# Optimization experiments

Hardware: AMD Instinct MI355X
Metric: run time of the kernel (lower is better)

The kernel has to match this reference:

```python
import jax, jax.numpy as jnp
import numpy as np

B, N = 8, 256          # trees per batch, nodes per tree
H, E, RD = 512, 512, 64  # hidden, word-embed, relation-embed dims
V, R = 32000, 64       # word vocab, relation vocab
SOS = 0                # SOS / null-token word id


def setup_inputs() -> dict:
    key = jax.random.key(0)
    ks = jax.random.split(key, 10)
    rng = np.random.default_rng(0)
    # topologically ordered tree: parent[i] < i, parent[0] = -1 (root -> encoder state)
    parent = np.full((N,), -1, dtype=np.int32)
    for i in range(1, N):
        parent[i] = rng.integers(0, i)
    s = 0.02
    return {
        "rel_ids": jax.random.randint(ks[0], (B, N), 0, R, dtype=jnp.int32),
        "sent_ids": jax.random.randint(ks[1], (B, N), 0, V, dtype=jnp.int32),
        "parent": jnp.asarray(parent),
        "root_h": jax.random.normal(ks[2], (B, H), jnp.float32),
        "word_emb": jax.random.normal(ks[3], (V, E), jnp.float32) * s,
        "rel_emb": jax.random.normal(ks[4], (R, RD), jnp.float32) * s,
        "Wx": jax.random.normal(ks[5], (RD + E, 4 * H), jnp.float32) * s,
        "Wh": jax.random.normal(ks[6], (H, 4 * H), jnp.float32) * s,
        "b": jnp.zeros((4 * H,), jnp.float32),
        "Wo": jax.random.normal(ks[7], (H, V), jnp.float32) * s,
        "bo": jnp.zeros((V,), jnp.float32),
    }


def reference(rel_ids, sent_ids, parent, root_h, word_emb, rel_emb, Wx, Wh, b, Wo, bo):
    Bd, Nd = rel_ids.shape
    Hd = root_h.shape[1]
    # word fed to each node = gold word of its parent (teacher forcing); SOS at root
    pidx = jnp.maximum(parent, 0)                           # [N]
    pword = jnp.where(parent[None, :] < 0, SOS, sent_ids[:, pidx])  # [B,N]
    x = jnp.concatenate([rel_emb[rel_ids], word_emb[pword]], axis=-1)  # [B,N,RD+E]
    Xg = jnp.einsum('bnd,dg->bng', x, Wx) + b               # precomputed input gates [B,N,4H]
    slot = parent + 1                                       # state-store slot (0 = root state)

    Hs0 = jnp.zeros((Bd, Nd + 1, Hd), Xg.dtype).at[:, 0].set(root_h)
    Cs0 = Hs0  # original sets cell state = hidden at the root

    def step(carry, inp):
        Hs, Cs = carry
        xg, sl, i = inp
        ph, pc = Hs[:, sl], Cs[:, sl]                       # parent state [B,H]
        g = xg + ph @ Wh                                    # [B,4H]
        ig, fg, og, gg = jnp.split(g, 4, axis=-1)
        c = jax.nn.sigmoid(fg) * pc + jax.nn.sigmoid(ig) * jnp.tanh(gg)
        h = jax.nn.sigmoid(og) * jnp.tanh(c)
        Hs = Hs.at[:, i + 1].set(h)
        Cs = Cs.at[:, i + 1].set(c)
        return (Hs, Cs), h

    xs = (Xg.transpose(1, 0, 2), slot, jnp.arange(Nd))
    (_, _), hs = jax.lax.scan(step, (Hs0, Cs0), xs)         # hs: [N,B,H]
    hs = hs.transpose(1, 0, 2)                              # [B,N,H]
    logits = jnp.einsum('bnh,hv->bnv', hs, Wo) + bo         # per-node vocab logits
    return logits
```

## Files before the change

kernel.cpp:

```cpp
#include <hip/hip_runtime.h>
#include <hip/hip_bf16.h>
#include <stdint.h>

#define BB 8
#define NN 256
#define HH 512
#define G4 2048
#define EE 512
#define RDIM 64
#define KX 576
#define VV 32000
#define SLICES 64
#define CSTRIDE 16

using f32x4 = __attribute__((ext_vector_type(4))) float;
using bf16x8 = __attribute__((ext_vector_type(8))) short;

__device__ __forceinline__ unsigned short f2bf(float f) {
  unsigned int u = __float_as_uint(f);
  u = (u + 0x7FFFu + ((u >> 16) & 1u)) >> 16;
  return (unsigned short)u;
}
__device__ __forceinline__ float bf2f(unsigned short s) {
  return __uint_as_float(((unsigned int)s) << 16);
}
__device__ __forceinline__ float sigm(float x) { return 1.0f / (1.0f + __expf(-x)); }

__global__ void init_kernel(const float* __restrict__ root_h, float* __restrict__ Hs,
                            float* __restrict__ Cs) {
  int i = blockIdx.x * 256 + threadIdx.x;
  float v = root_h[i];
  Hs[i] = v;
  Cs[i] = v;
}

__global__ __launch_bounds__(64) void levels_kernel(const int* __restrict__ parent,
                                                    int* __restrict__ order) {
  __shared__ int dep[NN];
  __shared__ int cnt[NN];
  int tid = threadIdx.x;
  for (int i = tid; i < NN; i += 64) cnt[i] = 0;
  __syncthreads();
  if (tid == 0) {
    for (int i = 0; i < NN; ++i) {
      int p = parent[i];
      int d = (p < 0) ? 0 : dep[p] + 1;
      dep[i] = d;
      cnt[d]++;
    }
    int run = 0;
    for (int d = 0; d < NN; ++d) { int c = cnt[d]; cnt[d] = run; run += c; }
    for (int i = 0; i < NN; ++i) order[cnt[dep[i]]++] = i;
  }
}

__global__ __launch_bounds__(256) void xg_kernel(
    const int* __restrict__ rel_ids, const int* __restrict__ sent_ids,
    const int* __restrict__ parent, const float* __restrict__ word_emb,
    const float* __restrict__ rel_emb, const float* __restrict__ Wx,
    const float* __restrict__ bias, float* __restrict__ Xg) {
  int n = blockIdx.y;
  int cb = blockIdx.x;
  int tid = threadIdx.x;
  __shared__ float xs[BB * KX];
  int par = parent[n];
  int b = tid >> 5;
  int l32 = tid & 31;
  int rid = rel_ids[b * NN + n];
  int pw = (par < 0) ? 0 : sent_ids[b * NN + par];
  const float* re = rel_emb + (size_t)rid * RDIM;
  const float* we = word_emb + (size_t)pw * EE;
  for (int q = l32; q < RDIM; q += 32) xs[b * KX + q] = re[q];
  for (int q = l32; q < EE; q += 32) xs[b * KX + RDIM + q] = we[q];
  __syncthreads();
  int col = cb * 256 + tid;
  float bb = bias[col];
  float acc[BB];
#pragma unroll
  for (int i = 0; i < BB; ++i) acc[i] = bb;
  const float* wxp = Wx + col;
  for (int k = 0; k < KX; k += 4) {
    float w0 = wxp[(size_t)(k + 0) * G4];
    float w1 = wxp[(size_t)(k + 1) * G4];
    float w2 = wxp[(size_t)(k + 2) * G4];
    float w3 = wxp[(size_t)(k + 3) * G4];
#pragma unroll
    for (int i = 0; i < BB; ++i) {
      f32x4 p = *(const f32x4*)&xs[i * KX + k];
      acc[i] = fmaf(p[0], w0, acc[i]);
      acc[i] = fmaf(p[1], w1, acc[i]);
      acc[i] = fmaf(p[2], w2, acc[i]);
      acc[i] = fmaf(p[3], w3, acc[i]);
    }
  }
  float* xgout = Xg + (size_t)n * (BB * G4) + col;
#pragma unroll
  for (int i = 0; i < BB; ++i) xgout[(size_t)i * G4] = acc[i];
}

__global__ __launch_bounds__(256) void wot_kernel(const float* __restrict__ Wo,
                                                  unsigned short* __restrict__ WoT) {
  __shared__ float t[64][65];
  int n0 = blockIdx.x * 64;
  int k0 = blockIdx.y * 64;
  int tid = threadIdx.x;
  int c = tid & 63;
  int r4 = tid >> 6;
#pragma unroll
  for (int i = 0; i < 16; ++i) {
    int r = r4 * 16 + i;
    t[r][c] = Wo[(size_t)(k0 + r) * VV + n0 + c];
  }
  __syncthreads();
#pragma unroll
  for (int i = 0; i < 16; ++i) {
    int nr = r4 * 16 + i;
    WoT[(size_t)(n0 + nr) * HH + k0 + c] = f2bf(t[c][nr]);
  }
}

__global__ __launch_bounds__(256, 3) void scan_kernel(
    const int* __restrict__ parent, const float* __restrict__ Wh,
    const float* __restrict__ Xg, float* Hs, float* Cs,
    unsigned short* __restrict__ hs_bf, const int* __restrict__ order,
    int* count, int* abortf, int ngroups) {
  int bid = blockIdx.x;
  int s = bid & 63;
  int g = bid >> 6;
  int tid = threadIdx.x;
  int lc = tid & 31;
  int kseg = tid >> 5;
  int b_ = tid >> 3, h_ = tid & 7;

  __shared__ __align__(16) unsigned short WhL[32 * 512];
  __shared__ __align__(16) float phL[BB * HH];

  for (int q = tid; q < 32 * 512; q += 256) {
    int k = q >> 5, c = q & 31;
    int gc = (c >> 3) * HH + s * 8 + (c & 7);
    WhL[((k >> 3) * 32 + c) * 8 + (k & 7)] = f2bf(Wh[(size_t)k * G4 + gc]);
  }
  __syncthreads();

  for (int idx = g; idx < NN; idx += ngroups) {
    int node = order[idx];
    int slot = parent[node] + 1;
    float xg4[4];
    if (tid < 64) {
#pragma unroll
      for (int gt = 0; gt < 4; ++gt)
        xg4[gt] = Xg[(size_t)node * (BB * G4) + (size_t)b_ * G4 + gt * HH + s * 8 + h_];
    }
    if (tid == 0 && slot > 0) {
      int v = 0;
      for (long spin = 0; spin < 150000L; ++spin) {
        v = __hip_atomic_load(&count[(size_t)(slot - 1) * CSTRIDE],
                              __ATOMIC_RELAXED, __HIP_MEMORY_SCOPE_AGENT);
        if (v == SLICES) break;
        if ((spin & 1023) == 1023) {
          if (__hip_atomic_load(abortf, __ATOMIC_RELAXED,
                                __HIP_MEMORY_SCOPE_AGENT) != 0) break;
        }
        __builtin_amdgcn_s_sleep(2);
      }
      if (v != SLICES) {
        __hip_atomic_store(abortf, 1, __ATOMIC_RELAXED, __HIP_MEMORY_SCOPE_AGENT);
      }
    }
    __syncthreads();

    {
      int b = tid >> 5, ko = (tid & 31) * 16;
      unsigned long long* src =
          (unsigned long long*)(Hs + (size_t)slot * (BB * HH) + b * HH + ko);
      float* d = &phL[b * HH + ko];
#pragma unroll
      for (int j = 0; j < 8; ++j) {
        unsigned long long v = __hip_atomic_load(&src[j], __ATOMIC_RELAXED,
                                                 __HIP_MEMORY_SCOPE_AGENT);
        d[2 * j] = __uint_as_float((unsigned int)v);
        d[2 * j + 1] = __uint_as_float((unsigned int)(v >> 32));
      }
    }
    __syncthreads();

    float acc[8];
#pragma unroll
    for (int b = 0; b < 8; ++b) acc[b] = 0.f;
    for (int k8 = 0; k8 < 8; ++k8) {
      int kg = kseg * 8 + k8;
      int kloc = kg * 8;
      bf16x8 wv = *(const bf16x8*)&WhL[(kg * 32 + lc) * 8];
      float wf[8];
#pragma unroll
      for (int j = 0; j < 8; ++j) wf[j] = bf2f((unsigned short)wv[j]);
#pragma unroll
      for (int b = 0; b < 8; ++b) {
        const float* pp = &phL[b * HH + kloc];
        f32x4 p0 = *(const f32x4*)pp;
        f32x4 p1 = *(const f32x4*)(pp + 4);
        acc[b] = fmaf(p0[0], wf[0], acc[b]);
        acc[b] = fmaf(p0[1], wf[1], acc[b]);
        acc[b] = fmaf(p0[2], wf[2], acc[b]);
        acc[b] = fmaf(p0[3], wf[3], acc[b]);
        acc[b] = fmaf(p1[0], wf[4], acc[b]);
        acc[b] = fmaf(p1[1], wf[5], acc[b]);
        acc[b] = fmaf(p1[2], wf[6], acc[b]);
        acc[b] = fmaf(p1[3], wf[7], acc[b]);
      }
    }
    __syncthreads();
    {
      float* part = phL;
      *(f32x4*)&part[tid * 8] = (f32x4){acc[0], acc[1], acc[2], acc[3]};
      *(f32x4*)&part[tid * 8 + 4] = (f32x4){acc[4], acc[5], acc[6], acc[7]};
    }
    __syncthreads();
    if (tid < 64) {
      const float* part = phL;
      float gsum[4];
#pragma unroll
      for (int gt = 0; gt < 4; ++gt) {
        int lc2 = gt * 8 + h_;
        float sm = xg4[gt];
#pragma unroll
        for (int q = 0; q < 8; ++q) sm += part[(q * 32 + lc2) * 8 + b_];
        gsum[gt] = sm;
      }
      int hidx = s * 8 + h_;
      float pc = __hip_atomic_load(&Cs[(size_t)slot * (BB * HH) + b_ * HH + hidx],
                                   __ATOMIC_RELAXED, __HIP_MEMORY_SCOPE_AGENT);
      float c = sigm(gsum[1]) * pc + sigm(gsum[0]) * tanhf(gsum[3]);
      float h = sigm(gsum[2]) * tanhf(c);
      size_t oi = (size_t)(node + 1) * (BB * HH) + b_ * HH + hidx;
      __hip_atomic_store(&Cs[oi], c, __ATOMIC_RELAXED, __HIP_MEMORY_SCOPE_AGENT);
      __hip_atomic_store(&Hs[oi], h, __ATOMIC_RELAXED, __HIP_MEMORY_SCOPE_AGENT);
      hs_bf[((size_t)b_ * NN + node) * HH + hidx] = f2bf(h);
    }
    if (tid == 0) {
      asm volatile("s_waitcnt vmcnt(0)" ::: "memory");
      __hip_atomic_fetch_add(&count[(size_t)node * CSTRIDE], 1, __ATOMIC_RELAXED,
                             __HIP_MEMORY_SCOPE_AGENT);
    }
    __syncthreads();
  }
}

__global__ __launch_bounds__(256) void gemm_kernel(
    const unsigned short* __restrict__ A, const unsigned short* __restrict__ Bt,
    const float* __restrict__ bo, float* __restrict__ C) {
  int bid = blockIdx.x;
  int swz = (bid & 7) * 500 + (bid >> 3);
  int nt = swz >> 4;
  int mt = swz & 15;
  int tid = threadIdx.x;
  int wave = tid >> 6;
  int lane = tid & 63;
  int wr = wave >> 1, wc = wave & 1;
  int lr = lane & 15, lh = lane >> 4;
  __shared__ __align__(16) unsigned short Al[128 * 32];
  __shared__ __align__(16) unsigned short Bl[128 * 32];
  int m0 = mt * 128, n0 = nt * 128;
  f32x4 acc[4][4];
#pragma unroll
  for (int i = 0; i < 4; ++i)
#pragma unroll
    for (int j = 0; j < 4; ++j) acc[i][j] = (f32x4){0.f, 0.f, 0.f, 0.f};

  for (int k0 = 0; k0 < HH; k0 += 32) {
#pragma unroll
    for (int q = 0; q < 2; ++q) {
      int off = wave * 2048 + q * 1024 + lane * 16;
      int r = off >> 6;
      int cb = off & 63;
      const unsigned short* ga = A + (size_t)(m0 + r) * HH + k0 + (cb >> 1);
      const unsigned short* gb = Bt + (size_t)(n0 + r) * HH + k0 + (cb >> 1);
      __builtin_amdgcn_global_load_lds(
          (const __attribute__((address_space(1))) unsigned int*)ga,
          (__attribute__((address_space(3))) unsigned int*)((char*)Al + wave * 2048 + q * 1024),
          16, 0, 0);
      __builtin_amdgcn_global_load_lds(
          (const __attribute__((address_space(1))) unsigned int*)gb,
          (__attribute__((address_space(3))) unsigned int*)((char*)Bl + wave * 2048 + q * 1024),
          16, 0, 0);
    }
    __syncthreads();
    bf16x8 af[4], bfr[4];
#pragma unroll
    for (int i = 0; i < 4; ++i) {
      af[i] = *(const bf16x8*)&Al[(wr * 64 + i * 16 + lr) * 32 + lh * 8];
      bfr[i] = *(const bf16x8*)&Bl[(wc * 64 + i * 16 + lr) * 32 + lh * 8];
    }
#pragma unroll
    for (int i = 0; i < 4; ++i)
#pragma unroll
      for (int j = 0; j < 4; ++j)
        acc[i][j] = __builtin_amdgcn_mfma_f32_16x16x32_bf16(af[i], bfr[j], acc[i][j], 0, 0, 0);
    __syncthreads();
  }
#pragma unroll
  for (int j = 0; j < 4; ++j) {
    int v = n0 + wc * 64 + j * 16 + lr;
    float bias = bo[v];
#pragma unroll
    for (int i = 0; i < 4; ++i) {
#pragma unroll
      for (int r2 = 0; r2 < 4; ++r2) {
        int m = m0 + wr * 64 + i * 16 + lh * 4 + r2;
        C[(size_t)m * VV + v] = acc[i][j][r2] + bias;
      }
    }
  }
}

static const size_t OFF_COUNT = 0;
static const size_t OFF_ABORT = 16384;
static const size_t OFF_ORDER = 16448;
static const size_t OFF_HS = 20480;
static const size_t OFF_CS = OFF_HS + 4210688;
static const size_t OFF_XG = OFF_CS + 4210688;
static const size_t OFF_HSBF = OFF_XG + 16777216;
static const size_t OFF_WOT = OFF_HSBF + 2097152;

extern "C" void kernel_launch(void* const* d_in, const int* in_sizes, int n_in,
                              void* d_out, int out_size, void* d_ws, size_t ws_size,
                              hipStream_t stream) {
  const int* rel_ids = (const int*)d_in[0];
  const int* sent_ids = (const int*)d_in[1];
  const int* parent = (const int*)d_in[2];
  const float* root_h = (const float*)d_in[3];
  const float* word_emb = (const float*)d_in[4];
  const float* rel_emb = (const float*)d_in[5];
  const float* Wx = (const float*)d_in[6];
  const float* Wh = (const float*)d_in[7];
  const float* bias = (const float*)d_in[8];
  const float* Wo = (const float*)d_in[9];
  const float* bo = (const float*)d_in[10];
  float* out = (float*)d_out;

  char* ws = (char*)d_ws;
  int* count = (int*)(ws + OFF_COUNT);
  int* abortf = (int*)(ws + OFF_ABORT);
  int* order = (int*)(ws + OFF_ORDER);
  float* Hs = (float*)(ws + OFF_HS);
  float* Cs = (float*)(ws + OFF_CS);
  float* Xg = (float*)(ws + OFF_XG);
  unsigned short* hs_bf = (unsigned short*)(ws + OFF_HSBF);
  unsigned short* WoT = (unsigned short*)(ws + OFF_WOT);

  hipMemsetAsync(ws, 0, 20480, stream);
  init_kernel<<<16, 256, 0, stream>>>(root_h, Hs, Cs);
  levels_kernel<<<1, 64, 0, stream>>>(parent, order);
  xg_kernel<<<dim3(8, 256), 256, 0, stream>>>(rel_ids, sent_ids, parent, word_emb,
                                              rel_emb, Wx, bias, Xg);
  wot_kernel<<<dim3(500, 8), 256, 0, stream>>>(Wo, WoT);
  {
    int ng = 12;
    void* args[] = {(void*)&parent, (void*)&Wh, (void*)&Xg, (void*)&Hs,
                    (void*)&Cs, (void*)&hs_bf, (void*)&order, (void*)&count,
                    (void*)&abortf, (void*)&ng};
    hipError_t e = hipLaunchCooperativeKernel((void*)scan_kernel, dim3(64 * 12),
                                              dim3(256), args, 0, stream);
    if (e != hipSuccess) {
      ng = 8;
      e = hipLaunchCooperativeKernel((void*)scan_kernel, dim3(64 * 8), dim3(256),
                                     args, 0, stream);
      if (e != hipSuccess) {
        scan_kernel<<<512, 256, 0, stream>>>(parent, Wh, Xg, Hs, Cs, hs_bf,
                                             order, count, abortf, 8);
      }
    }
  }
  gemm_kernel<<<4000, 256, 0, stream>>>(hs_bf, WoT, bo, out);
}
```

Measured before the change: 758.5 us.

## Deepen GEMM K-tile, XOR-swizzle LDS, and transpose MFMA for vectorized stores

The logits GEMM now loads 64-wide K tiles per iteration, which halves the number of barrier pairs. LDS rows use an XOR swizzle on 16-byte chunks to avoid bank conflicts on fragment reads. The MFMA operands are swapped so each lane holds four consecutive vocab columns, allowing 16-byte vector stores of the output and a vector bias load instead of scalar strided stores. LDS use doubles, which may reduce occupancy.

New measurement: 772.1 us. Within noise of the previous version (+1.8%).

```diff
diff --git a/kernel.cpp b/kernel.cpp
--- a/kernel.cpp
+++ b/kernel.cpp
@@ -258,57 +258,65 @@
   int lane = tid & 63;
   int wr = wave >> 1, wc = wave & 1;
   int lr = lane & 15, lh = lane >> 4;
-  __shared__ __align__(16) unsigned short Al[128 * 32];
-  __shared__ __align__(16) unsigned short Bl[128 * 32];
+  __shared__ __align__(16) unsigned short Al[128 * 64];
+  __shared__ __align__(16) unsigned short Bl[128 * 64];
   int m0 = mt * 128, n0 = nt * 128;
   f32x4 acc[4][4];
 #pragma unroll
-  for (int i = 0; i < 4; ++i)
-#pragma unroll
-    for (int j = 0; j < 4; ++j) acc[i][j] = (f32x4){0.f, 0.f, 0.f, 0.f};
-
-  for (int k0 = 0; k0 < HH; k0 += 32) {
-#pragma unroll
-    for (int q = 0; q < 2; ++q) {
-      int off = wave * 2048 + q * 1024 + lane * 16;
-      int r = off >> 6;
-      int cb = off & 63;
-      const unsigned short* ga = A + (size_t)(m0 + r) * HH + k0 + (cb >> 1);
-      const unsigned short* gb = Bt + (size_t)(n0 + r) * HH + k0 + (cb >> 1);
+  for (int j = 0; j < 4; ++j)
+#pragma unroll
+    for (int i = 0; i < 4; ++i) acc[j][i] = (f32x4){0.f, 0.f, 0.f, 0.f};
+
+  for (int k0 = 0; k0 < HH; k0 += 64) {
+#pragma unroll
+    for (int q = 0; q < 4; ++q) {
+      int gI = q * 256 + tid;
+      int r = gI >> 3;
+      int ch = (gI & 7) ^ (r & 7);
+      const unsigned short* ga = A + (size_t)(m0 + r) * HH + k0 + ch * 8;
+      const unsigned short* gb = Bt + (size_t)(n0 + r) * HH + k0 + ch * 8;
       __builtin_amdgcn_global_load_lds(
           (const __attribute__((address_space(1))) unsigned int*)ga,
-          (__attribute__((address_space(3))) unsigned int*)((char*)Al + wave * 2048 + q * 1024),
+          (__attribute__((address_space(3))) unsigned int*)((char*)Al + q * 4096 + wave * 1024),
           16, 0, 0);
       __builtin_amdgcn_global_load_lds(
           (const __attribute__((address_space(1))) unsigned int*)gb,
-          (__attribute__((address_space(3))) unsigned int*)((char*)Bl + wave * 2048 + q * 1024),
+          (__attribute__((address_space(3))) unsigned int*)((char*)Bl + q * 4096 + wave * 1024),
           16, 0, 0);
     }
     __syncthreads();
-    bf16x8 af[4], bfr[4];
+#pragma unroll
+    for (int ks = 0; ks < 2; ++ks) {
+      bf16x8 af[4], bfr[4];
+#pragma unroll
+      for (int i = 0; i < 4; ++i) {
+        int ra = wr * 64 + i * 16 + lr;
+        af[i] = *(const bf16x8*)&Al[ra * 64 + (((ks * 4 + lh) ^ (ra & 7)) * 8)];
+        int rb = wc * 64 + i * 16 + lr;
+        bfr[i] = *(const bf16x8*)&Bl[rb * 64 + (((ks * 4 + lh) ^ (rb & 7)) * 8)];
+      }
+#pragma unroll
+      for (int j = 0; j < 4; ++j)
+#pragma unroll
+        for (int i = 0; i < 4; ++i)
+          acc[j][i] = __builtin_amdgcn_mfma_f32_16x16x32_bf16(bfr[j], af[i],
+                                                              acc[j][i], 0, 0, 0);
+    }
+    __syncthreads();
+  }
+#pragma unroll
+  for (int j = 0; j < 4; ++j) {
+    int vb = n0 + wc * 64 + j * 16 + lh * 4;
+    f32x4 bv = *(const f32x4*)&bo[vb];
 #pragma unroll
     for (int i = 0; i < 4; ++i) {
-      af[i] = *(const bf16x8*)&Al[(wr * 64 + i * 16 + lr) * 32 + lh * 8];
-      bfr[i] = *(const bf16x8*)&Bl[(wc * 64 + i * 16 + lr) * 32 + lh * 8];
-    }
-#pragma unroll
-    for (int i = 0; i < 4; ++i)
-#pragma unroll
-      for (int j = 0; j < 4; ++j)
-        acc[i][j] = __builtin_amdgcn_mfma_f32_16x16x32_bf16(af[i], bfr[j], acc[i][j], 0, 0, 0);
-    __syncthreads();
-  }
-#pragma unroll
-  for (int j = 0; j < 4; ++j) {
-    int v = n0 + wc * 64 + j * 16 + lr;
-    float bias = bo[v];
-#pragma unroll
-    for (int i = 0; i < 4; ++i) {
-#pragma unroll
-      for (int r2 = 0; r2 < 4; ++r2) {
-        int m = m0 + wr * 64 + i * 16 + lh * 4 + r2;
-        C[(size_t)m * VV + v] = acc[i][j][r2] + bias;
-      }
+      int m = m0 + wr * 64 + i * 16 + lr;
+      f32x4 o;
+      o[0] = acc[j][i][0] + bv[0];
+      o[1] = acc[j][i][1] + bv[1];
+      o[2] = acc[j][i][2] + bv[2];
+      o[3] = acc[j][i][3] + bv[3];
+      *(f32x4*)&C[(size_t)m * VV + vb] = o;
     }
   }
 }
```
